# Optimization experiments

Measured on AMD Instinct MI355X. Metric: run time of the kernel, lower is better.

Reference implementation:

```python
import jax, jax.numpy as jnp
import numpy as np

B, DM, H, W = 2, 96, 48, 48
E = 192          # d_expand == d_inner
R, N = 6, 16     # delta_rank, d_state


def conv2d(x, w, b, groups=1, pad=0):
    out = jax.lax.conv_general_dilated(
        x, w, window_strides=(1, 1), padding=[(pad, pad), (pad, pad)],
        dimension_numbers=("NCHW", "OIHW", "NCHW"), feature_group_count=groups)
    return out + b[None, :, None, None]


def setup_inputs() -> dict:
    key = jax.random.key(0)
    ks = jax.random.split(key, 24)
    f = lambda k, shape, s: jax.random.normal(k, shape, jnp.float32) * s
    inp = {
        "x": jax.random.normal(ks[0], (B, DM, H, W), jnp.float32),
        "in_proj_w": f(ks[1], (2 * E, DM), 0.05),
        "conv_w": f(ks[2], (E, 1, 3, 3), 0.2),
        "conv_b": f(ks[3], (E,), 0.1),
        "x_proj_w": f(ks[4], (4, R + 2 * N, E), 0.01),
        "dt_proj_w": f(ks[5], (4, E, R), 0.01),
        "dt_proj_b": jnp.full((4, E), -9.0) + f(ks[6], (4, E), 0.1),
        "A_log": jnp.tile(jnp.log(jnp.arange(1, N + 1, dtype=jnp.float32))[None, None, :], (4, E, 1)),
        "Ds": jnp.ones((4, E), jnp.float32),
        "ln_g": jnp.ones(E, jnp.float32), "ln_b": jnp.zeros(E, jnp.float32),
        "c1_w": f(ks[7], (2 * E, E, 1, 1), 0.05), "c1_b": jnp.zeros(2 * E),
        "bn1_g": jnp.ones(2 * E), "bn1_b": jnp.zeros(2 * E), "bn1_m": jnp.zeros(2 * E), "bn1_v": jnp.ones(2 * E),
        "c2_w": f(ks[8], (2 * E, 1, 3, 3), 0.2), "c2_b": jnp.zeros(2 * E),
        "bn2_g": jnp.ones(2 * E), "bn2_b": jnp.zeros(2 * E), "bn2_m": jnp.zeros(2 * E), "bn2_v": jnp.ones(2 * E),
        "c3_w": f(ks[9], (E // 2, 2 * E, 1, 1), 0.05), "c3_b": jnp.zeros(E // 2),
        "se1_w": f(ks[10], (E // 4, E // 2), 0.1), "se1_b": jnp.zeros(E // 4),
        "se2_w": f(ks[11], (E // 2, E // 4), 0.1), "se2_b": jnp.zeros(E // 2),
    }
    return inp


def reference(x, in_proj_w, conv_w, conv_b, x_proj_w, dt_proj_w, dt_proj_b,
              A_log, Ds, ln_g, ln_b,
              c1_w, c1_b, bn1_g, bn1_b, bn1_m, bn1_v,
              c2_w, c2_b, bn2_g, bn2_b, bn2_m, bn2_v,
              c3_w, c3_b, se1_w, se1_b, se2_w, se2_b):
    Bs, _, Hs, Ws = x.shape
    L = Hs * Ws
    # in projection (Linear over channel dim), split x/z gates
    xz = jnp.einsum("bchw,oc->bohw", x, in_proj_w)
    xi, z = jnp.split(xz, 2, axis=1)
    # depthwise conv + SiLU
    xi = jax.nn.silu(conv2d(xi, conv_w, conv_b, groups=E, pad=1))
    # ---- selective scan (4-direction cross scan, cumsum formulation) ----
    xf = xi.reshape(Bs, E, L)
    xt = jnp.swapaxes(xi, 2, 3).reshape(Bs, E, L)
    xs = jnp.stack([xf, xf[..., ::-1], xt, xt[..., ::-1]], axis=1)  # [B,4,E,L]
    dbc = jnp.einsum("bkcl,krc->bkrl", xs, x_proj_w)                # [B,4,R+2N,L]
    dlt, b, c = dbc[:, :, :R], dbc[:, :, R:R + N], dbc[:, :, R + N:]
    dlt = jnp.einsum("bkrl,kdr->bkdl", dlt, dt_proj_w) + dt_proj_b[None, :, :, None]
    dlt = jax.nn.softplus(dlt)                                      # [B,4,E,L]
    dA = dlt[..., None] * A_log[None, :, :, None, :]                # [B,4,E,L,N]
    phi = jnp.exp(-jnp.cumsum(dA, axis=3))
    dbx = dlt[..., None] * jnp.swapaxes(b, 2, 3)[:, :, None] * xs[..., None]  # [B,4,E,L,N]
    h = phi * jnp.cumsum(dbx / (phi + 1e-12), axis=3)
    y = jnp.einsum("bkdln,bknl->bkdl", h, c) + Ds[None, :, :, None]  # [B,4,E,L]
    # ---- cross merge ----
    y1 = y[:, 0]
    y2 = y[:, 1, :, ::-1]
    y3 = jnp.swapaxes(y[:, 2].reshape(Bs, E, Ws, Hs), 2, 3).reshape(Bs, E, L)
    y4 = jnp.swapaxes(y[:, 3, :, ::-1].reshape(Bs, E, Ws, Hs), 2, 3).reshape(Bs, E, L)
    ys = (y1 + y2 + y3 + y4).reshape(Bs, E, Hs, Ws)
    # layernorm over channels
    yn = jnp.moveaxis(ys, 1, -1)
    mu = yn.mean(-1, keepdims=True)
    var = yn.var(-1, keepdims=True)
    yn = (yn - mu) / jnp.sqrt(var + 1e-5) * ln_g + ln_b
    u = jnp.moveaxis(yn, -1, 1) * z
    # ---- EFFN ----
    def bn(t, g, bb, m, v):
        return (t - m[None, :, None, None]) / jnp.sqrt(v + 1e-5)[None, :, None, None] * g[None, :, None, None] + bb[None, :, None, None]
    t = jax.nn.relu(bn(conv2d(u, c1_w, c1_b), bn1_g, bn1_b, bn1_m, bn1_v))
    t = jax.nn.relu(bn(conv2d(t, c2_w, c2_b, groups=2 * E, pad=1), bn2_g, bn2_b, bn2_m, bn2_v))
    t = conv2d(t, c3_w, c3_b)
    # squeeze-excitation: t + t * sigmoid(fc(relu(fc(avgpool(t)))))
    s = t.mean((2, 3))
    s = jax.nn.relu(s @ se1_w.T + se1_b)
    s = jax.nn.sigmoid(s @ se2_w.T + se2_b)
    return t + t * s[:, :, None, None]
```

## Files before the change

### kernel.cpp

```cpp
#include <hip/hip_runtime.h>
#include <hip/hip_bf16.h>

#define LTOT 2304
#define ECH  192
#define NCH  16
#define CCH  192
#define SCH  12

__device__ __forceinline__ int permS(int k, int l) {
  if (k == 0) return l;
  if (k == 1) return LTOT - 1 - l;
  int m = (k == 2) ? l : (LTOT - 1 - l);
  return (m % 48) * 48 + (m / 48);
}

__device__ __forceinline__ float sp_fast(float x) {
  float t = __expf(x);
  return (t <= 0.018f) ? t * fmaf(t, fmaf(t, 0.33333334f, -0.5f), 1.f) : log1pf(t);
}

__global__ __launch_bounds__(256) void k1_inproj(const float* __restrict__ x,
                                                 const float* __restrict__ W,
                                                 float* __restrict__ xi_pre,
                                                 float* __restrict__ z) {
  const int l0 = blockIdx.x * 32;
  const int o0 = blockIdx.y * 64;
  const int b  = blockIdx.z;
  __shared__ __align__(16) float xs[96 * 34];
  __shared__ __align__(16) float Wl[96 * 68];
  const int tid = threadIdx.x;
  for (int idx = tid; idx < 96 * 32; idx += 256) {
    int i = idx & 31, cc = idx >> 5;
    xs[cc * 34 + i] = x[(b * 96 + cc) * LTOT + l0 + i];
  }
  for (int idx = tid; idx < 96 * 16; idx += 256) {
    int cc = idx % 96, rq = idx / 96;
    float4 v;
    v.x = W[(o0 + 4 * rq + 0) * 96 + cc];
    v.y = W[(o0 + 4 * rq + 1) * 96 + cc];
    v.z = W[(o0 + 4 * rq + 2) * 96 + cc];
    v.w = W[(o0 + 4 * rq + 3) * 96 + cc];
    *(float4*)&Wl[cc * 68 + 4 * rq] = v;
  }
  __syncthreads();
  const int lane = tid & 63, w = tid >> 6;
  const int jj = lane & 15, rqq = lane >> 4;
  const int rbase = 16 * w + 4 * rqq;
  float acc[2][4];
#pragma unroll
  for (int p = 0; p < 2; ++p)
#pragma unroll
    for (int t = 0; t < 4; ++t) acc[p][t] = 0.f;
#pragma unroll 4
  for (int cc = 0; cc < 96; ++cc) {
    const float4 wv = *(const float4*)&Wl[cc * 68 + rbase];
    const float2 xv = *(const float2*)&xs[cc * 34 + 2 * jj];
    acc[0][0] = fmaf(wv.x, xv.x, acc[0][0]); acc[0][1] = fmaf(wv.y, xv.x, acc[0][1]);
    acc[0][2] = fmaf(wv.z, xv.x, acc[0][2]); acc[0][3] = fmaf(wv.w, xv.x, acc[0][3]);
    acc[1][0] = fmaf(wv.x, xv.y, acc[1][0]); acc[1][1] = fmaf(wv.y, xv.y, acc[1][1]);
    acc[1][2] = fmaf(wv.z, xv.y, acc[1][2]); acc[1][3] = fmaf(wv.w, xv.y, acc[1][3]);
  }
  __syncthreads();
  float* ol = xs;
#pragma unroll
  for (int t = 0; t < 4; ++t) {
    ol[(rbase + t) * 33 + 2 * jj]     = acc[0][t];
    ol[(rbase + t) * 33 + 2 * jj + 1] = acc[1][t];
  }
  __syncthreads();
  for (int idx = tid; idx < 32 * 64; idx += 256) {
    int r = idx & 63, pos = idx >> 6;
    float v = ol[r * 33 + pos];
    int o = o0 + r, l = l0 + pos;
    if (o < ECH) xi_pre[(b * LTOT + l) * ECH + o] = v;
    else         z[(b * LTOT + l) * ECH + (o - ECH)] = v;
  }
}

__global__ __launch_bounds__(256) void k2_dwconv(const float4* __restrict__ xi_pre4,
                                                 const float* __restrict__ cw,
                                                 const float* __restrict__ cb,
                                                 float4* __restrict__ xi4) {
  int g = blockIdx.x * 256 + threadIdx.x;
  if (g >= 2 * LTOT * 48) return;
  int e4 = g % 48; int l = (g / 48) % LTOT; int b = g / (48 * LTOT);
  int h = l / 48, wq = l % 48;
  int e0 = 4 * e4;
  float wt[4][9];
#pragma unroll
  for (int j = 0; j < 4; ++j)
#pragma unroll
    for (int t = 0; t < 9; ++t) wt[j][t] = cw[(e0 + j) * 9 + t];
  float4 acc = *(const float4*)&cb[e0];
#pragma unroll
  for (int kh = 0; kh < 3; ++kh) {
    int hh = h + kh - 1; if (hh < 0 || hh >= 48) continue;
#pragma unroll
    for (int kw = 0; kw < 3; ++kw) {
      int ww = wq + kw - 1; if (ww < 0 || ww >= 48) continue;
      float4 v = xi_pre4[(b * LTOT + hh * 48 + ww) * 48 + e4];
      int t = kh * 3 + kw;
// ... 6 lines not shown
  acc.x = acc.x / (1.f + __expf(-acc.x));
  acc.y = acc.y / (1.f + __expf(-acc.y));
  acc.z = acc.z / (1.f + __expf(-acc.z));
  acc.w = acc.w / (1.f + __expf(-acc.w));
  xi4[g] = acc;
}

__global__ __launch_bounds__(256) void k3_xproj(const float* __restrict__ xi,
                                                const float* __restrict__ xw,
                                                float* __restrict__ dl6g,
                                                float* __restrict__ bT,
                                                float* __restrict__ cT) {
  const int l0 = blockIdx.x * 32;
  const int k  = blockIdx.y;
  const int b  = blockIdx.z;
  __shared__ __align__(16) float xs[96 * 34];
  __shared__ __align__(16) float Wl[192 * 44];
  const int tid = threadIdx.x;
  const float* wsrc = xw + k * 38 * ECH;
  for (int idx = tid; idx < 38 * 192; idx += 256) {
    int r = idx / 192, cc = idx - r * 192;
    Wl[cc * 44 + r] = wsrc[idx];
  }
  const int lane = tid & 63, w = tid >> 6;
  const int jj = lane & 15;
  const int rq = w * 4 + (lane >> 4);
  const int rqc = rq < 9 ? rq : 9;
  const int j0 = 2 * jj;
  float a00 = 0.f, a01 = 0.f, a02 = 0.f, a03 = 0.f;
  float a10 = 0.f, a11 = 0.f, a12 = 0.f, a13 = 0.f;
  for (int kc = 0; kc < 2; ++kc) {
    __syncthreads();
    for (int idx = tid; idx < 32 * 96; idx += 256) {
      int j = idx / 96, cc = idx - j * 96;
      int s = permS(k, l0 + j);
      xs[cc * 34 + j] = xi[(b * LTOT + s) * ECH + kc * 96 + cc];
    }
    __syncthreads();
#pragma unroll 4
    for (int cc = 0; cc < 96; ++cc) {
      const float2 xv = *(const float2*)&xs[cc * 34 + j0];
      const float4 wv = *(const float4*)&Wl[(kc * 96 + cc) * 44 + 4 * rqc];
      a00 = fmaf(wv.x, xv.x, a00); a01 = fmaf(wv.y, xv.x, a01);
      a02 = fmaf(wv.z, xv.x, a02); a03 = fmaf(wv.w, xv.x, a03);
      a10 = fmaf(wv.x, xv.y, a10); a11 = fmaf(wv.y, xv.y, a11);
      a12 = fmaf(wv.z, xv.y, a12); a13 = fmaf(wv.w, xv.y, a13);
    }
  }
  const int bk = b * 4 + k;
  if (rq < 10) {
    float av[2][4] = {{a00, a01, a02, a03}, {a10, a11, a12, a13}};
#pragma unroll
    for (int t = 0; t < 4; ++t) {
      int r = 4 * rq + t;
      if (r >= 38) continue;
#pragma unroll
      for (int p = 0; p < 2; ++p) {
        int j = j0 + p;
        float v = av[p][t];
        if (r < 6)       dl6g[((bk * LTOT) + l0 + j) * 6 + r] = v;
        else if (r < 22) bT[((bk * LTOT) + l0 + j) * NCH + (r - 6)] = v;
        else             cT[((bk * LTOT) + l0 + j) * NCH + (r - 22)] = v;
      }
    }
  }
}

__global__ __launch_bounds__(256) void k4a_scan1(const float* __restrict__ dl6g,
                                                 const float* __restrict__ xi,
                                                 const float* __restrict__ bT,
                                                 const float* __restrict__ Alog,
                                                 const float* __restrict__ dtw,
                                                 const float* __restrict__ dtb,
                                                 float* __restrict__ q,
                                                 float* __restrict__ Ts) {
  const int cb = blockIdx.x;
  const int db = blockIdx.y;
  const int bk = blockIdx.z;
  const int b = bk >> 2, k = bk & 3;
  const int l0 = cb * 48;
  __shared__ __align__(16) float2 sdx[48 * 64];
  __shared__ __align__(16) float  sb[48 * NCH];
  const int tid = threadIdx.x;
  const int dd = tid & 63, cg = tid >> 6;
  const int dg = db * 64 + dd;
  float b6 = dtb[k * ECH + dg];
  float w6[6];
  {
    const float2* d2 = (const float2*)(dtw + (k * ECH + dg) * 6);
    float2 u0 = d2[0], u1 = d2[1], u2 = d2[2];
    w6[0] = u0.x; w6[1] = u0.y; w6[2] = u1.x; w6[3] = u1.y; w6[4] = u2.x; w6[5] = u2.y;
  }
  for (int idx = tid; idx < 48 * NCH; idx += 256) sb[idx] = bT[(bk * LTOT + l0) * NCH + idx];
  for (int e = tid; e < 48 * 64; e += 256) {
    int s = e >> 6;
    const float* d6 = dl6g + (bk * LTOT + l0 + s) * 6;
    float xa = b6;
#pragma unroll
    for (int r = 0; r < 6; ++r) xa = fmaf(w6[r], d6[r], xa);
    float dl = sp_fast(xa);
    int sp = permS(k, l0 + s);
    sdx[s * 64 + dd] = make_float2(dl, dl * xi[(b * LTOT + sp) * ECH + dg]);
  }
  float C1[16], h[16];
#pragma unroll
  for (int n = 0; n < 16; ++n) {
    C1[n] = Alog[(k * ECH + dg) * NCH + n];
    h[n] = 0.f;
  }
  __syncthreads();
  float Tsum = 0.f;
  for (int i = 0; i < SCH; ++i) {
    int j = cg * SCH + i;
    float2 dx = sdx[j * 64 + dd];
    float dl = dx.x;
    float u  = dx.y;
    Tsum += dl;
    const float4* bb4 = (const float4*)(sb + j * NCH);
    float4 q0 = bb4[0], q1 = bb4[1], q2 = bb4[2], q3 = bb4[3];
    float bbl[16] = {q0.x, q0.y, q0.z, q0.w, q1.x, q1.y, q1.z, q1.w,
                     q2.x, q2.y, q2.z, q2.w, q3.x, q3.y, q3.z, q3.w};
    if (dl <= 0.018f) {
#pragma unroll
      for (int n = 0; n < 16; ++n) {
        float xn = C1[n] * dl;
        float e = fmaf(xn, fmaf(xn, fmaf(xn, -(1.f / 6.f), 0.5f), -1.f), 1.f);
        h[n] = fmaf(e, h[n], u * bbl[n]);
      }
    } else {
#pragma unroll
      for (int n = 0; n < 16; ++n) {
        float e = __expf(-C1[n] * dl);
        h[n] = fmaf(e, h[n], u * bbl[n]);
      }
    }
  }
  const int c = cb * 4 + cg;
  float4* qp = (float4*)(q + ((bk * CCH + c) * ECH + dg) * NCH);
  qp[0] = make_float4(h[0], h[1], h[2], h[3]);
  qp[1] = make_float4(h[4], h[5], h[6], h[7]);
  qp[2] = make_float4(h[8], h[9], h[10], h[11]);
  qp[3] = make_float4(h[12], h[13], h[14], h[15]);
  Ts[(bk * CCH + c) * ECH + dg] = Tsum;
}

__global__ __launch_bounds__(256) void k4b_comb(const float* __restrict__ Alog,
                                                const float* __restrict__ Ts,
                                                float* __restrict__ q) {
  const int d  = blockIdx.x;
  const int bk = blockIdx.y;
  const int k  = bk & 3;
  const int tid = threadIdx.x;
  const int n = tid & 15, seg = tid >> 4;
  const float A = Alog[(k * ECH + d) * NCH + n];
  const int c0 = seg * 12;
  const float* tb = Ts + (bk * CCH + c0) * ECH + d;
  float* qp = q + ((bk * CCH + c0) * ECH + d) * NCH + n;
  float qv[12], P[12];
#pragma unroll
  for (int i = 0; i < 12; ++i) qv[i] = qp[i * (ECH * NCH)];
#pragma unroll
  for (int i = 0; i < 12; ++i) {
    float xv = A * tb[i * ECH];
    P[i] = (xv <= 0.05f)
               ? fmaf(xv, fmaf(xv, fmaf(xv, -(1.f / 6.f), 0.5f), -1.f), 1.f)
               : __expf(-xv);
  }
  float hl = 0.f, Pp = 1.f;
#pragma unroll
  for (int i = 0; i < 12; ++i) { hl = fmaf(P[i], hl, qv[i]); Pp *= P[i]; }
  __shared__ float2 comb[16][17];
  comb[seg][n] = make_float2(Pp, hl);
  __syncthreads();
  float H = 0.f;
  for (int s = 0; s < seg; ++s) {
    float2 cb = comb[s][n];
    H = fmaf(cb.x, H, cb.y);
  }
  float h = H;
#pragma unroll
  for (int i = 0; i < 12; ++i) {
    float hp = h;
    h = fmaf(P[i], h, qv[i]);
    qp[i * (ECH * NCH)] = hp;
  }
}

__global__ __launch_bounds__(256) void k4c_scan2(const float* __restrict__ dl6g,
                                                 const float* __restrict__ xi,
                                                 const float* __restrict__ bT,
                                                 const float* __restrict__ cT,
                                                 const float* __restrict__ Alog,
                                                 const float* __restrict__ dtw,
                                                 const float* __restrict__ dtb,
                                                 const float* __restrict__ hin,
                                                 float* __restrict__ ys) {
  const int cb = blockIdx.x;
  const int db = blockIdx.y;
  const int bk = blockIdx.z;
  const int b = bk >> 2, k = bk & 3;
  const int l0 = cb * 48;
  __shared__ __align__(16) float2 sdx[48 * 64];
  __shared__ __align__(16) float  sb[48 * NCH];
  __shared__ __align__(16) float  sc[48 * NCH];
  const int tid = threadIdx.x;
  const int dd = tid & 63, cg = tid >> 6;
  const int dg = db * 64 + dd;
  float b6 = dtb[k * ECH + dg];
  float w6[6];
  {
    const float2* d2 = (const float2*)(dtw + (k * ECH + dg) * 6);
    float2 u0 = d2[0], u1 = d2[1], u2 = d2[2];
    w6[0] = u0.x; w6[1] = u0.y; w6[2] = u1.x; w6[3] = u1.y; w6[4] = u2.x; w6[5] = u2.y;
  }
  for (int idx = tid; idx < 48 * NCH; idx += 256) {
    sb[idx] = bT[(bk * LTOT + l0) * NCH + idx];
    sc[idx] = cT[(bk * LTOT + l0) * NCH + idx];
  }
  for (int e = tid; e < 48 * 64; e += 256) {
    int s = e >> 6;
    const float* d6 = dl6g + (bk * LTOT + l0 + s) * 6;
    float xa = b6;
#pragma unroll
    for (int r = 0; r < 6; ++r) xa = fmaf(w6[r], d6[r], xa);
    float dl = sp_fast(xa);
    int sp = permS(k, l0 + s);
    sdx[s * 64 + dd] = make_float2(dl, dl * xi[(b * LTOT + sp) * ECH + dg]);
  }
  float C1[16], h[16];
  const int c = cb * 4 + cg;
  const float4* hp = (const float4*)(hin + ((bk * CCH + c) * ECH + dg) * NCH);
  {
    float4 h0 = hp[0], h1 = hp[1], h2 = hp[2], h3 = hp[3];
    h[0]=h0.x; h[1]=h0.y; h[2]=h0.z; h[3]=h0.w;
    h[4]=h1.x; h[5]=h1.y; h[6]=h1.z; h[7]=h1.w;
    h[8]=h2.x; h[9]=h2.y; h[10]=h2.z; h[11]=h2.w;
    h[12]=h3.x; h[13]=h3.y; h[14]=h3.z; h[15]=h3.w;
  }
#pragma unroll
  for (int n = 0; n < 16; ++n) C1[n] = Alog[(k * ECH + dg) * NCH + n];
  __syncthreads();
  for (int i = 0; i < SCH; ++i) {
    int j = cg * SCH + i;
    float2 dx = sdx[j * 64 + dd];
    float dl = dx.x;
    float u  = dx.y;
    const float4* bb4 = (const float4*)(sb + j * NCH);
    float4 q0 = bb4[0], q1 = bb4[1], q2 = bb4[2], q3 = bb4[3];
    float bbl[16] = {q0.x, q0.y, q0.z, q0.w, q1.x, q1.y, q1.z, q1.w,
                     q2.x, q2.y, q2.z, q2.w, q3.x, q3.y, q3.z, q3.w};
    if (dl <= 0.018f) {
#pragma unroll
      for (int n = 0; n < 16; ++n) {
        float xn = C1[n] * dl;
        float e = fmaf(xn, fmaf(xn, fmaf(xn, -(1.f / 6.f), 0.5f), -1.f), 1.f);
        h[n] = fmaf(e, h[n], u * bbl[n]);
      }
    } else {
#pragma unroll
      for (int n = 0; n < 16; ++n) {
        float e = __expf(-C1[n] * dl);
        h[n] = fmaf(e, h[n], u * bbl[n]);
      }
    }
    const float4* cc4 = (const float4*)(sc + j * NCH);
    float4 c0 = cc4[0], c1 = cc4[1], c2 = cc4[2], c3 = cc4[3];
    float ccl[16] = {c0.x, c0.y, c0.z, c0.w, c1.x, c1.y, c1.z, c1.w,
                     c2.x, c2.y, c2.z, c2.w, c3.x, c3.y, c3.z, c3.w};
    float y = 0.f;
#pragma unroll
    for (int n = 0; n < 16; ++n) y = fmaf(h[n], ccl[n], y);
    int sp = permS(k, l0 + j);
    atomicAdd(&ys[(b * LTOT + sp) * ECH + dg], y);
  }
}

__global__ __launch_bounds__(256) void k5_ln(const float* __restrict__ ys,
                                             const float* __restrict__ Ds,
                                             const float* __restrict__ lng,
                                             const float* __restrict__ lnb,
                                             float* __restrict__ zu) {
  int p = blockIdx.x * 4 + (threadIdx.x >> 6);
  int lane = threadIdx.x & 63;
  const float* yp = ys + p * ECH;
  float vd[3], sd[3];
#pragma unroll
  for (int t = 0; t < 3; ++t) {
    int d = lane + t * 64;
    vd[t] = yp[d];
    sd[t] = Ds[d] + Ds[ECH + d] + Ds[2 * ECH + d] + Ds[3 * ECH + d];
  }
  float s1 = vd[0] + vd[1] + vd[2];
  float s2 = sd[0] + sd[1] + sd[2];
#pragma unroll
  for (int off = 32; off > 0; off >>= 1) {
    s1 += __shfl_xor(s1, off, 64);
    s2 += __shfl_xor(s2, off, 64);
  }
  float mean_dot = s1 * (1.f / 192.f);
  float mean_sd  = s2 * (1.f / 192.f);
  float dev[3];
  float ss = 0.f;
#pragma unroll
  for (int t = 0; t < 3; ++t) {
    dev[t] = (vd[t] - mean_dot) + (sd[t] - mean_sd);
    ss = fmaf(dev[t], dev[t], ss);
  }
#pragma unroll
  for (int off = 32; off > 0; off >>= 1) ss += __shfl_xor(ss, off, 64);
  float rstd = 1.f / sqrtf(ss * (1.f / 192.f) + 1e-5f);
#pragma unroll
  for (int t = 0; t < 3; ++t) {
    int d = lane + t * 64;
    float yn = (dev[t] * rstd) * lng[d] + lnb[d];
    zu[p * ECH + d] = yn * zu[p * ECH + d];
  }
}

__global__ __launch_bounds__(256) void k6_c1(const float* __restrict__ u,
                                             const float* __restrict__ W,
                                             const float* __restrict__ c1b,
                                             const float* __restrict__ g1,
                                             const float* __restrict__ b1,
                                             const float* __restrict__ m1,
                                             const float* __restrict__ v1,
                                             float* __restrict__ t1,
                                             float* __restrict__ se) {
  const int l0 = blockIdx.x * 32;
  const int o0 = blockIdx.y * 64;
// ... 159 lines not shown
}

__global__ __launch_bounds__(256) void k9_out(const float* __restrict__ t3,
                                              const float* __restrict__ se,
                                              const float* __restrict__ w1,
                                              const float* __restrict__ sb1,
                                              const float* __restrict__ w2,
                                              const float* __restrict__ sb2,
                                              float* __restrict__ out) {
  __shared__ float sm[192];
  __shared__ float s1[96];
  __shared__ float smul[192];
  int t = threadIdx.x;
  if (t < 192) sm[t] = se[t] * (1.f / 2304.f);
  __syncthreads();
  if (t < 96) {
    int b = t / 48, i = t % 48;
    float a = sb1[i];
#pragma unroll 4
    for (int m = 0; m < 96; ++m) a = fmaf(w1[i * 96 + m], sm[b * 96 + m], a);
    s1[t] = fmaxf(a, 0.f);
  }
  __syncthreads();
  if (t < 192) {
    int b = t / 96, j = t % 96;
    float a = sb2[j];
#pragma unroll 4
    for (int i = 0; i < 48; ++i) a = fmaf(w2[j * 48 + i], s1[b * 48 + i], a);
    smul[t] = 1.f + 1.f / (1.f + __expf(-a));
  }
  __syncthreads();
  int g = blockIdx.x * 256 + t;
  if (g < 2 * 96 * LTOT) out[g] = t3[g] * smul[g / LTOT];
}

extern "C" void kernel_launch(void* const* d_in, const int* in_sizes, int n_in,
                              void* d_out, int out_size, void* d_ws, size_t ws_size,
                              hipStream_t stream) {
  const float* x     = (const float*)d_in[0];
  const float* inw   = (const float*)d_in[1];
  const float* convw = (const float*)d_in[2];
  const float* convb = (const float*)d_in[3];
  const float* xpw   = (const float*)d_in[4];
  const float* dtw   = (const float*)d_in[5];
  const float* dtb   = (const float*)d_in[6];
  const float* Alog  = (const float*)d_in[7];
  const float* Ds    = (const float*)d_in[8];
  const float* lng   = (const float*)d_in[9];
  const float* lnb   = (const float*)d_in[10];
  const float* c1w   = (const float*)d_in[11];
  const float* c1b   = (const float*)d_in[12];
  const float* bn1g  = (const float*)d_in[13];
  const float* bn1b  = (const float*)d_in[14];
  const float* bn1m  = (const float*)d_in[15];
  const float* bn1v  = (const float*)d_in[16];
  const float* c2w   = (const float*)d_in[17];
  const float* c2b   = (const float*)d_in[18];
  const float* bn2g  = (const float*)d_in[19];
  const float* bn2b  = (const float*)d_in[20];
  const float* bn2m  = (const float*)d_in[21];
  const float* bn2v  = (const float*)d_in[22];
  const float* c3w   = (const float*)d_in[23];
  const float* c3b   = (const float*)d_in[24];
  const float* se1w  = (const float*)d_in[25];
  const float* se1b  = (const float*)d_in[26];
  const float* se2w  = (const float*)d_in[27];
  const float* se2b  = (const float*)d_in[28];

  float* ws = (float*)d_ws;
  float* xi_pre = ws;
  float* z      = ws + 884736;
  float* xi     = ws + 1769472;
  float* dl6g   = ws + 2654208;
  float* bT     = ws + 2764800;
  float* cT     = ws + 3354624;
  float* q      = ws + 3944448;
  float* Ts     = ws + 13381632;
  float* se     = ws + 13676544;
  float* ys     = ws + 13676736;
  float* t1 = q;
  float* t2 = q + 1769472;
  float* t3 = q + 3538944;

  hipMemsetAsync(ys, 0, 884736 * sizeof(float), stream);

  k1_inproj<<<dim3(72, 6, 2), 256, 0, stream>>>(x, inw, xi_pre, z);
  k2_dwconv<<<864, 256, 0, stream>>>((const float4*)xi_pre, convw, convb, (float4*)xi);
  k3_xproj<<<dim3(72, 4, 2), 256, 0, stream>>>(xi, xpw, dl6g, bT, cT);
  k4a_scan1<<<dim3(48, 3, 8), 256, 0, stream>>>(dl6g, xi, bT, Alog, dtw, dtb, q, Ts);
  k4b_comb<<<dim3(192, 8), 256, 0, stream>>>(Alog, Ts, q);
  k4c_scan2<<<dim3(48, 3, 8), 256, 0, stream>>>(dl6g, xi, bT, cT, Alog, dtw, dtb, q, ys);
  k5_ln<<<1152, 256, 0, stream>>>(ys, Ds, lng, lnb, z);
  k6_c1<<<dim3(72, 6, 2), 256, 0, stream>>>(z, c1w, c1b, bn1g, bn1b, bn1m, bn1v, t1, se);
  k7_dw2<<<1728, 256, 0, stream>>>(t1, c2w, c2b, bn2g, bn2b, bn2m, bn2v, t2);
  k8_c3<<<dim3(72, 3, 2), 256, 0, stream>>>(t2, c3w, c3b, t3, se);
  k9_out<<<1728, 256, 0, stream>>>(t3, se, se1w, se1b, se2w, se2b, (float*)d_out);
}
```

Measured before the change: 291.7 us.

## Fuse all stages into one cooperative persistent kernel with grid syncs

Replaces the eleven-kernel launch chain with a single cooperative persistent kernel that walks every stage in grid-stride loops separated by grid-wide barriers. The goal is to remove per-launch overhead and the gaps between kernels, and it also zeroes the ys buffer inside the kernel instead of issuing a memset. The scan chunking changes from 192 chunks of 12 to 144 chunks of 16 steps, processed in two halves through shared memory. Grid syncs cost time of their own, the grid is capped at 1024 blocks, and the multi-kernel path remains as a fallback if the cooperative launch fails.

```diff
diff --git a/kernel.cpp b/kernel.cpp
--- a/kernel.cpp
+++ b/kernel.cpp
@@ -1,11 +1,15 @@
 #include <hip/hip_runtime.h>
 #include <hip/hip_bf16.h>
+#include <hip/hip_cooperative_groups.h>
+
+namespace cg = cooperative_groups;
 
 #define LTOT 2304
 #define ECH  192
 #define NCH  16
 #define CCH  192
 #define SCH  12
+#define MCCH 144
 
 __device__ __forceinline__ int permS(int k, int l) {
   if (k == 0) return l;
@@ -17,6 +21,614 @@
 __device__ __forceinline__ float sp_fast(float x) {
   float t = __expf(x);
   return (t <= 0.018f) ? t * fmaf(t, fmaf(t, 0.33333334f, -0.5f), 1.f) : log1pf(t);
+}
+
+struct MParams {
+  const float *x, *inw, *convw, *convb, *xpw, *dtw, *dtb, *Alog, *Ds, *lng, *lnb;
+  const float *c1w, *c1b, *bn1g, *bn1b, *bn1m, *bn1v;
+  const float *c2w, *c2b, *bn2g, *bn2b, *bn2m, *bn2v;
+  const float *c3w, *c3b, *se1w, *se1b, *se2w, *se2b;
+  float *xi_pre, *z, *xi, *dl6g, *bT, *cT, *q, *Ts, *se, *ys, *out;
+};
+
+__global__ __launch_bounds__(256, 4) void mega(MParams P) {
+  cg::grid_group gridg = cg::this_grid();
+  __shared__ __align__(16) unsigned char smem[39168];
+  const int tid = threadIdx.x;
+  const int bid = blockIdx.x;
+  const int nbl = gridDim.x;
+  const int lane = tid & 63, wv_ = tid >> 6;
+  const int jj = lane & 15, rqq = lane >> 4;
+
+  if (bid == 0 && tid < 192) P.se[tid] = 0.f;
+  {
+    float* xs = (float*)smem;
+    float* Wl = (float*)smem + 96 * 34;
+    const int rbase = 16 * wv_ + 4 * rqq;
+    for (int u = bid; u < 864; u += nbl) {
+      int b = u / 432, rem = u - b * 432;
+      int oy = rem / 72, lb = rem - oy * 72;
+      int l0 = lb * 32, o0 = oy * 64;
+      for (int idx = tid; idx < 96 * 32; idx += 256) {
+        int i = idx & 31, cc = idx >> 5;
+        xs[cc * 34 + i] = P.x[(b * 96 + cc) * LTOT + l0 + i];
+      }
+      for (int idx = tid; idx < 96 * 16; idx += 256) {
+        int cc = idx % 96, rq = idx / 96;
+        float4 v;
+        v.x = P.inw[(o0 + 4 * rq + 0) * 96 + cc];
+        v.y = P.inw[(o0 + 4 * rq + 1) * 96 + cc];
+        v.z = P.inw[(o0 + 4 * rq + 2) * 96 + cc];
+        v.w = P.inw[(o0 + 4 * rq + 3) * 96 + cc];
+        *(float4*)&Wl[cc * 68 + 4 * rq] = v;
+      }
+      __syncthreads();
+      float acc[2][4];
+#pragma unroll
+      for (int p = 0; p < 2; ++p)
+#pragma unroll
+        for (int t = 0; t < 4; ++t) acc[p][t] = 0.f;
+#pragma unroll 4
+      for (int cc = 0; cc < 96; ++cc) {
+        const float4 wv = *(const float4*)&Wl[cc * 68 + rbase];
+        const float2 xv = *(const float2*)&xs[cc * 34 + 2 * jj];
+        acc[0][0] = fmaf(wv.x, xv.x, acc[0][0]); acc[0][1] = fmaf(wv.y, xv.x, acc[0][1]);
+        acc[0][2] = fmaf(wv.z, xv.x, acc[0][2]); acc[0][3] = fmaf(wv.w, xv.x, acc[0][3]);
+        acc[1][0] = fmaf(wv.x, xv.y, acc[1][0]); acc[1][1] = fmaf(wv.y, xv.y, acc[1][1]);
+        acc[1][2] = fmaf(wv.z, xv.y, acc[1][2]); acc[1][3] = fmaf(wv.w, xv.y, acc[1][3]);
+      }
+      __syncthreads();
+      float* ol = xs;
+#pragma unroll
+      for (int t = 0; t < 4; ++t) {
+        ol[(rbase + t) * 33 + 2 * jj]     = acc[0][t];
+        ol[(rbase + t) * 33 + 2 * jj + 1] = acc[1][t];
+      }
+      __syncthreads();
+      for (int idx = tid; idx < 32 * 64; idx += 256) {
+        int r = idx & 63, pos = idx >> 6;
+        float v = ol[r * 33 + pos];
+        int o = o0 + r, l = l0 + pos;
+        if (o < ECH) P.xi_pre[(b * LTOT + l) * ECH + o] = v;
+        else         P.z[(b * LTOT + l) * ECH + (o - ECH)] = v;
+      }
+      __syncthreads();
+    }
+  }
+  gridg.sync();
+
+  {
+    const float4* src4 = (const float4*)P.xi_pre;
+    float4* dst4 = (float4*)P.xi;
+    for (int v2 = bid; v2 < 864; v2 += nbl) {
+      int g = v2 * 256 + tid;
+      int e4 = g % 48; int l = (g / 48) % LTOT; int b = g / (48 * LTOT);
+      int h = l / 48, wq = l % 48;
+      int e0 = 4 * e4;
+      float wt[4][9];
+#pragma unroll
+      for (int j2 = 0; j2 < 4; ++j2)
+#pragma unroll
+        for (int t = 0; t < 9; ++t) wt[j2][t] = P.convw[(e0 + j2) * 9 + t];
+      float4 acc = *(const float4*)&P.convb[e0];
+#pragma unroll
+      for (int kh = 0; kh < 3; ++kh) {
+        int hh = h + kh - 1; if (hh < 0 || hh >= 48) continue;
+#pragma unroll
+        for (int kw = 0; kw < 3; ++kw) {
+          int ww = wq + kw - 1; if (ww < 0 || ww >= 48) continue;
+          float4 v = src4[(b * LTOT + hh * 48 + ww) * 48 + e4];
+          int t = kh * 3 + kw;
+          acc.x = fmaf(wt[0][t], v.x, acc.x);
+          acc.y = fmaf(wt[1][t], v.y, acc.y);
+          acc.z = fmaf(wt[2][t], v.z, acc.z);
+          acc.w = fmaf(wt[3][t], v.w, acc.w);
+        }
+      }
+      acc.x = acc.x / (1.f + __expf(-acc.x));
+      acc.y = acc.y / (1.f + __expf(-acc.y));
+      acc.z = acc.z / (1.f + __expf(-acc.z));
+      acc.w = acc.w / (1.f + __expf(-acc.w));
+      dst4[g] = acc;
+    }
+  }
+  gridg.sync();
+
+  {
+    for (int i = bid * 256 + tid; i < 221184; i += nbl * 256)
+      ((float4*)P.ys)[i] = make_float4(0.f, 0.f, 0.f, 0.f);
+    float* xs = (float*)smem;
+    float* Wl = (float*)smem + 96 * 34;
+    for (int u = bid; u < 576; u += nbl) {
+      int b = u / 288, rem = u - b * 288;
+      int k = rem / 72, lb = rem - k * 72;
+      int l0 = lb * 32;
+      const int rq = wv_ * 4 + rqq;
+      const int rqc = rq < 9 ? rq : 9;
+      const int j0 = 2 * jj;
+      float a00 = 0.f, a01 = 0.f, a02 = 0.f, a03 = 0.f;
+      float a10 = 0.f, a11 = 0.f, a12 = 0.f, a13 = 0.f;
+      for (int kc = 0; kc < 2; ++kc) {
+        __syncthreads();
+        for (int idx = tid; idx < 32 * 96; idx += 256) {
+          int j = idx / 96, cc = idx - j * 96;
+          int s = permS(k, l0 + j);
+          xs[cc * 34 + j] = P.xi[(b * LTOT + s) * ECH + kc * 96 + cc];
+        }
+        for (int idx = tid; idx < 38 * 96; idx += 256) {
+          int r = idx / 96, cc = idx - r * 96;
+          Wl[cc * 44 + r] = P.xpw[(k * 38 + r) * ECH + kc * 96 + cc];
+        }
+        __syncthreads();
+#pragma unroll 4
+        for (int cc = 0; cc < 96; ++cc) {
+          const float2 xv = *(const float2*)&xs[cc * 34 + j0];
+          const float4 wvv = *(const float4*)&Wl[cc * 44 + 4 * rqc];
+          a00 = fmaf(wvv.x, xv.x, a00); a01 = fmaf(wvv.y, xv.x, a01);
+          a02 = fmaf(wvv.z, xv.x, a02); a03 = fmaf(wvv.w, xv.x, a03);
+          a10 = fmaf(wvv.x, xv.y, a10); a11 = fmaf(wvv.y, xv.y, a11);
+          a12 = fmaf(wvv.z, xv.y, a12); a13 = fmaf(wvv.w, xv.y, a13);
+        }
+      }
+      const int bk = b * 4 + k;
+      if (rq < 10) {
+        float av[2][4] = {{a00, a01, a02, a03}, {a10, a11, a12, a13}};
+#pragma unroll
+        for (int t = 0; t < 4; ++t) {
+          int r = 4 * rq + t;
+          if (r >= 38) continue;
+#pragma unroll
+          for (int p = 0; p < 2; ++p) {
+            int j = j0 + p;
+            float v = av[p][t];
+            if (r < 6)       P.dl6g[((bk * LTOT) + l0 + j) * 6 + r] = v;
+            else if (r < 22) P.bT[((bk * LTOT) + l0 + j) * NCH + (r - 6)] = v;
+            else             P.cT[((bk * LTOT) + l0 + j) * NCH + (r - 22)] = v;
+          }
+        }
+      }
+      __syncthreads();
+    }
+  }
+  gridg.sync();
+
+  {
+    float*  sb  = (float*)smem;
+    float2* sdx = (float2*)((float*)smem + 1024);
+    for (int u = bid; u < 864; u += nbl) {
+      int bk = u / 108, r1 = u - bk * 108;
+      int db = r1 / 36, lb = r1 - db * 36;
+      int b = bk >> 2, k = bk & 3;
+      int l0 = lb * 64;
+      int dd = lane, cgw = wv_;
+      int dg = db * 64 + dd;
+      float b6 = P.dtb[k * ECH + dg];
+      float w6[6];
+      {
+        const float2* d2 = (const float2*)(P.dtw + (k * ECH + dg) * 6);
+        float2 u0 = d2[0], u1 = d2[1], u2 = d2[2];
+        w6[0] = u0.x; w6[1] = u0.y; w6[2] = u1.x; w6[3] = u1.y; w6[4] = u2.x; w6[5] = u2.y;
+      }
+      for (int idx = tid; idx < 64 * NCH; idx += 256)
+        sb[idx] = P.bT[(bk * LTOT + l0) * NCH + idx];
+      float C1[16], h[16];
+#pragma unroll
+      for (int n = 0; n < 16; ++n) {
+        C1[n] = P.Alog[(k * ECH + dg) * NCH + n];
+        h[n] = 0.f;
+      }
+      float Tsum = 0.f;
+      for (int hf = 0; hf < 2; ++hf) {
+        __syncthreads();
+        for (int e = tid; e < 32 * 64; e += 256) {
+          int s = e >> 6;
+          int j = (s >> 3) * 16 + hf * 8 + (s & 7);
+          const float* d6 = P.dl6g + (bk * LTOT + l0 + j) * 6;
+          float xa = b6;
+#pragma unroll
+          for (int r = 0; r < 6; ++r) xa = fmaf(w6[r], d6[r], xa);
+          float dl = sp_fast(xa);
+          int sp = permS(k, l0 + j);
+          sdx[s * 64 + dd] = make_float2(dl, dl * P.xi[(b * LTOT + sp) * ECH + dg]);
+        }
+        __syncthreads();
+        for (int i = 0; i < 8; ++i) {
+          int j = cgw * 16 + hf * 8 + i;
+          float2 dx = sdx[(cgw * 8 + i) * 64 + dd];
+          float dl = dx.x, uu = dx.y;
+          Tsum += dl;
+          const float4* bb4 = (const float4*)(sb + j * NCH);
+          float4 q0 = bb4[0], q1 = bb4[1], q2 = bb4[2], q3 = bb4[3];
+          float bbl[16] = {q0.x, q0.y, q0.z, q0.w, q1.x, q1.y, q1.z, q1.w,
+                           q2.x, q2.y, q2.z, q2.w, q3.x, q3.y, q3.z, q3.w};
+          if (dl <= 0.018f) {
+#pragma unroll
+            for (int n = 0; n < 16; ++n) {
+              float xn = C1[n] * dl;
+              float e = fmaf(xn, fmaf(xn, fmaf(xn, -(1.f / 6.f), 0.5f), -1.f), 1.f);
+              h[n] = fmaf(e, h[n], uu * bbl[n]);
+            }
+          } else {
+#pragma unroll
+            for (int n = 0; n < 16; ++n) {
+              float e = __expf(-C1[n] * dl);
+              h[n] = fmaf(e, h[n], uu * bbl[n]);
+            }
+          }
+        }
+      }
+      int c = lb * 4 + cgw;
+      float4* qp = (float4*)(P.q + ((bk * MCCH + c) * ECH + dg) * NCH);
+      qp[0] = make_float4(h[0], h[1], h[2], h[3]);
+      qp[1] = make_float4(h[4], h[5], h[6], h[7]);
+      qp[2] = make_float4(h[8], h[9], h[10], h[11]);
+      qp[3] = make_float4(h[12], h[13], h[14], h[15]);
+      P.Ts[(bk * MCCH + c) * ECH + dg] = Tsum;
+      __syncthreads();
+    }
+  }
+  gridg.sync();
+
+  {
+    float2 (*comb)[17] = (float2(*)[17])smem;
+    for (int u = bid; u < 768; u += nbl) {
+      int bk = u / 96, dp = u - bk * 96;
+      int k = bk & 3;
+      for (int dloc = 0; dloc < 2; ++dloc) {
+        int d = dp * 2 + dloc;
+        int n = tid & 15, seg = tid >> 4;
+        float A = P.Alog[(k * ECH + d) * NCH + n];
+        int c0 = seg * 9;
+        const float* tb = P.Ts + (bk * MCCH + c0) * ECH + d;
+        float* qp = P.q + ((bk * MCCH + c0) * ECH + d) * NCH + n;
+        float qv[9], Pl[9];
+#pragma unroll
+        for (int i = 0; i < 9; ++i) qv[i] = qp[i * (ECH * NCH)];
+#pragma unroll
+        for (int i = 0; i < 9; ++i) {
+          float xv = A * tb[i * ECH];
+          Pl[i] = (xv <= 0.05f)
+                      ? fmaf(xv, fmaf(xv, fmaf(xv, -(1.f / 6.f), 0.5f), -1.f), 1.f)
+                      : __expf(-xv);
+        }
+        float hl = 0.f, Pp = 1.f;
+#pragma unroll
+        for (int i = 0; i < 9; ++i) { hl = fmaf(Pl[i], hl, qv[i]); Pp *= Pl[i]; }
+        comb[seg][n] = make_float2(Pp, hl);
+        __syncthreads();
+        float H = 0.f;
+        for (int s2 = 0; s2 < seg; ++s2) {
+          float2 cb = comb[s2][n];
+          H = fmaf(cb.x, H, cb.y);
+        }
+        float h = H;
+#pragma unroll
+        for (int i = 0; i < 9; ++i) {
+          float hp = h;
+          h = fmaf(Pl[i], h, qv[i]);
+          qp[i * (ECH * NCH)] = hp;
+        }
+        __syncthreads();
+      }
+    }
+  }
+  gridg.sync();
+
+  {
+    float*  sb  = (float*)smem;
+    float*  sc  = (float*)smem + 1024;
+    float2* sdx = (float2*)((float*)smem + 2048);
+    for (int u = bid; u < 864; u += nbl) {
+      int bk = u / 108, r1 = u - bk * 108;
+      int db = r1 / 36, lb = r1 - db * 36;
+      int b = bk >> 2, k = bk & 3;
+      int l0 = lb * 64;
+      int dd = lane, cgw = wv_;
+      int dg = db * 64 + dd;
+      float b6 = P.dtb[k * ECH + dg];
+      float w6[6];
+      {
+        const float2* d2 = (const float2*)(P.dtw + (k * ECH + dg) * 6);
+        float2 u0 = d2[0], u1 = d2[1], u2 = d2[2];
+        w6[0] = u0.x; w6[1] = u0.y; w6[2] = u1.x; w6[3] = u1.y; w6[4] = u2.x; w6[5] = u2.y;
+      }
+      for (int idx = tid; idx < 64 * NCH; idx += 256) {
+        sb[idx] = P.bT[(bk * LTOT + l0) * NCH + idx];
+        sc[idx] = P.cT[(bk * LTOT + l0) * NCH + idx];
+      }
+      int c = lb * 4 + cgw;
+      float C1[16], h[16];
+      const float4* hp4 = (const float4*)(P.q + ((bk * MCCH + c) * ECH + dg) * NCH);
+      {
+        float4 h0 = hp4[0], h1 = hp4[1], h2 = hp4[2], h3 = hp4[3];
+        h[0]=h0.x; h[1]=h0.y; h[2]=h0.z; h[3]=h0.w;
+        h[4]=h1.x; h[5]=h1.y; h[6]=h1.z; h[7]=h1.w;
+        h[8]=h2.x; h[9]=h2.y; h[10]=h2.z; h[11]=h2.w;
+        h[12]=h3.x; h[13]=h3.y; h[14]=h3.z; h[15]=h3.w;
+      }
+#pragma unroll
+      for (int n = 0; n < 16; ++n) C1[n] = P.Alog[(k * ECH + dg) * NCH + n];
+      for (int hf = 0; hf < 2; ++hf) {
+        __syncthreads();
+        for (int e = tid; e < 32 * 64; e += 256) {
+          int s = e >> 6;
+          int j = (s >> 3) * 16 + hf * 8 + (s & 7);
+          const float* d6 = P.dl6g + (bk * LTOT + l0 + j) * 6;
+          float xa = b6;
+#pragma unroll
+          for (int r = 0; r < 6; ++r) xa = fmaf(w6[r], d6[r], xa);
+          float dl = sp_fast(xa);
+          int sp = permS(k, l0 + j);
+          sdx[s * 64 + dd] = make_float2(dl, dl * P.xi[(b * LTOT + sp) * ECH + dg]);
+        }
+        __syncthreads();
+        for (int i = 0; i < 8; ++i) {
+          int j = cgw * 16 + hf * 8 + i;
+          float2 dx = sdx[(cgw * 8 + i) * 64 + dd];
+          float dl = dx.x, uu = dx.y;
+          const float4* bb4 = (const float4*)(sb + j * NCH);
+          float4 q0 = bb4[0], q1 = bb4[1], q2 = bb4[2], q3 = bb4[3];
+          float bbl[16] = {q0.x, q0.y, q0.z, q0.w, q1.x, q1.y, q1.z, q1.w,
+                           q2.x, q2.y, q2.z, q2.w, q3.x, q3.y, q3.z, q3.w};
+          if (dl <= 0.018f) {
+#pragma unroll
+            for (int n = 0; n < 16; ++n) {
+              float xn = C1[n] * dl;
+              float e = fmaf(xn, fmaf(xn, fmaf(xn, -(1.f / 6.f), 0.5f), -1.f), 1.f);
+              h[n] = fmaf(e, h[n], uu * bbl[n]);
+            }
+          } else {
+#pragma unroll
+            for (int n = 0; n < 16; ++n) {
+              float e = __expf(-C1[n] * dl);
+              h[n] = fmaf(e, h[n], uu * bbl[n]);
+            }
+          }
+          const float4* cc4 = (const float4*)(sc + j * NCH);
+          float4 c0v = cc4[0], c1v = cc4[1], c2v = cc4[2], c3v = cc4[3];
+          float ccl[16] = {c0v.x, c0v.y, c0v.z, c0v.w, c1v.x, c1v.y, c1v.z, c1v.w,
+                           c2v.x, c2v.y, c2v.z, c2v.w, c3v.x, c3v.y, c3v.z, c3v.w};
+          float y = 0.f;
+#pragma unroll
+          for (int n = 0; n < 16; ++n) y = fmaf(h[n], ccl[n], y);
+          int sp = permS(k, j + l0);
+          atomicAdd(&P.ys[(b * LTOT + sp) * ECH + dg], y);
+        }
+      }
+      __syncthreads();
+    }
+  }
+  gridg.sync();
+
+  {
+    for (int v2 = bid; v2 < 1152; v2 += nbl) {
+      int p = v2 * 4 + wv_;
+      const float* yp = P.ys + p * ECH;
+      float vd[3], sd[3];
+#pragma unroll
+      for (int t = 0; t < 3; ++t) {
+        int d = lane + t * 64;
+        vd[t] = yp[d];
+        sd[t] = P.Ds[d] + P.Ds[ECH + d] + P.Ds[2 * ECH + d] + P.Ds[3 * ECH + d];
+      }
+      float s1 = vd[0] + vd[1] + vd[2];
+      float s2 = sd[0] + sd[1] + sd[2];
+#pragma unroll
+      for (int off = 32; off > 0; off >>= 1) {
+        s1 += __shfl_xor(s1, off, 64);
+        s2 += __shfl_xor(s2, off, 64);
+      }
+      float mean_dot = s1 * (1.f / 192.f);
+      float mean_sd  = s2 * (1.f / 192.f);
+      float dev[3];
+      float ss = 0.f;
+#pragma unroll
+      for (int t = 0; t < 3; ++t) {
+        dev[t] = (vd[t] - mean_dot) + (sd[t] - mean_sd);
+        ss = fmaf(dev[t], dev[t], ss);
+      }
+#pragma unroll
+      for (int off = 32; off > 0; off >>= 1) ss += __shfl_xor(ss, off, 64);
+      float rstd = 1.f / sqrtf(ss * (1.f / 192.f) + 1e-5f);
+#pragma unroll
+      for (int t = 0; t < 3; ++t) {
+        int d = lane + t * 64;
+        float yn = (dev[t] * rstd) * P.lng[d] + P.lnb[d];
+        P.z[p * ECH + d] = yn * P.z[p * ECH + d];
+      }
+    }
+  }
+  gridg.sync();
+
+  {
+    float* xs = (float*)smem;
+    float* Wl = (float*)smem + 96 * 34;
+    float* t1 = P.q;
+    const int rbase = 16 * wv_ + 4 * rqq;
+    for (int u = bid; u < 864; u += nbl) {
+      int b = u / 432, rem = u - b * 432;
+      int oy = rem / 72, lb = rem - oy * 72;
+      int l0 = lb * 32, o0 = oy * 64;
+      float acc[2][4];
+#pragma unroll
+      for (int p = 0; p < 2; ++p)
+#pragma unroll
+        for (int t = 0; t < 4; ++t) acc[p][t] = 0.f;
+      for (int kc = 0; kc < 2; ++kc) {
+        __syncthreads();
+        for (int idx = tid; idx < 32 * 96; idx += 256) {
+          int cc = idx % 96, i = idx / 96;
+          xs[cc * 34 + i] = P.z[(b * LTOT + l0 + i) * ECH + kc * 96 + cc];
+        }
+        for (int idx = tid; idx < 96 * 16; idx += 256) {
+          int cc = idx % 96, rq = idx / 96;
+          float4 v;
+          v.x = P.c1w[(o0 + 4 * rq + 0) * ECH + kc * 96 + cc];
+          v.y = P.c1w[(o0 + 4 * rq + 1) * ECH + kc * 96 + cc];
+          v.z = P.c1w[(o0 + 4 * rq + 2) * ECH + kc * 96 + cc];
+          v.w = P.c1w[(o0 + 4 * rq + 3) * ECH + kc * 96 + cc];
+          *(float4*)&Wl[cc * 68 + 4 * rq] = v;
+        }
+        __syncthreads();
+#pragma unroll 4
+        for (int cc = 0; cc < 96; ++cc) {
+          const float4 wv = *(const float4*)&Wl[cc * 68 + rbase];
+          const float2 xv = *(const float2*)&xs[cc * 34 + 2 * jj];
+          acc[0][0] = fmaf(wv.x, xv.x, acc[0][0]); acc[0][1] = fmaf(wv.y, xv.x, acc[0][1]);
+          acc[0][2] = fmaf(wv.z, xv.x, acc[0][2]); acc[0][3] = fmaf(wv.w, xv.x, acc[0][3]);
+          acc[1][0] = fmaf(wv.x, xv.y, acc[1][0]); acc[1][1] = fmaf(wv.y, xv.y, acc[1][1]);
+          acc[1][2] = fmaf(wv.z, xv.y, acc[1][2]); acc[1][3] = fmaf(wv.w, xv.y, acc[1][3]);
+        }
+      }
+#pragma unroll
+      for (int t = 0; t < 4; ++t) {
+        int o = o0 + rbase + t;
+        float sc2 = P.bn1g[o] / sqrtf(P.bn1v[o] + 1e-5f);
+        float bias = (P.c1b[o] - P.bn1m[o]) * sc2 + P.bn1b[o];
+#pragma unroll
+        for (int p = 0; p < 2; ++p) acc[p][t] = fmaxf(fmaf(acc[p][t], sc2, bias), 0.f);
+      }
+      __syncthreads();
+      float* ol = xs;
+#pragma unroll
+      for (int t = 0; t < 4; ++t) {
+        ol[(rbase + t) * 33 + 2 * jj]     = acc[0][t];
+        ol[(rbase + t) * 33 + 2 * jj + 1] = acc[1][t];
+      }
+      __syncthreads();
+      for (int idx = tid; idx < 32 * 64; idx += 256) {
+        int pos = idx & 31, r = idx >> 5;
+        t1[(b * 384 + o0 + r) * LTOT + l0 + pos] = ol[r * 33 + pos];
+      }
+      __syncthreads();
+    }
+  }
+  gridg.sync();
+
+  {
+    const float* t1 = P.q;
+    float* t2 = P.q + 1769472;
+    for (int v2 = bid; v2 < 1728; v2 += nbl) {
+      int g = v2 * 256 + tid;
+      int p = g % 576; int o = (g / 576) % 384; int b = g / (576 * 384);
+      int l0 = 4 * p; int h = l0 / 48; int wq0 = l0 % 48;
+      const float* src = t1 + (b * 384 + o) * LTOT;
+      float wt[9];
+#pragma unroll
+      for (int t = 0; t < 9; ++t) wt[t] = P.c2w[o * 9 + t];
+      float bias0 = P.c2b[o];
+      float4 a = make_float4(bias0, bias0, bias0, bias0);
+#pragma unroll
+      for (int kh = 0; kh < 3; ++kh) {
+        int hh = h + kh - 1; if (hh < 0 || hh >= 48) continue;
+        const float* row = src + hh * 48;
+        float4 c = *(const float4*)(row + wq0);
+        float lft = (wq0 > 0)  ? row[wq0 - 1] : 0.f;
+        float rgt = (wq0 < 44) ? row[wq0 + 4] : 0.f;
+        float w0 = wt[kh * 3], w1 = wt[kh * 3 + 1], w2 = wt[kh * 3 + 2];
+        a.x = fmaf(w0, lft, fmaf(w1, c.x, fmaf(w2, c.y, a.x)));
+        a.y = fmaf(w0, c.x, fmaf(w1, c.y, fmaf(w2, c.z, a.y)));
+        a.z = fmaf(w0, c.y, fmaf(w1, c.z, fmaf(w2, c.w, a.z)));
+        a.w = fmaf(w0, c.z, fmaf(w1, c.w, fmaf(w2, rgt, a.w)));
+      }
+      float sc2 = P.bn2g[o] / sqrtf(P.bn2v[o] + 1e-5f);
+      float bs = (0.f - P.bn2m[o]) * sc2 + P.bn2b[o];
+      a.x = fmaxf(fmaf(a.x, sc2, bs), 0.f);
+      a.y = fmaxf(fmaf(a.y, sc2, bs), 0.f);
+      a.z = fmaxf(fmaf(a.z, sc2, bs), 0.f);
+      a.w = fmaxf(fmaf(a.w, sc2, bs), 0.f);
+      *(float4*)(t2 + (b * 384 + o) * LTOT + l0) = a;
+    }
+  }
+  gridg.sync();
+
+  {
+    float* xs = (float*)smem;
+    float* Wl = (float*)smem + 96 * 34;
+    const float* t2 = P.q + 1769472;
+    float* t3 = P.q + 3538944;
+    const int rloc = 8 * wv_ + 2 * rqq;
+    for (int u = bid; u < 432; u += nbl) {
+      int b = u / 216, rem = u - b * 216;
+      int ry = rem / 72, lb = rem - ry * 72;
+      int l0 = lb * 32, r0 = ry * 32;
+      float acc[2][2];
+      acc[0][0] = acc[0][1] = acc[1][0] = acc[1][1] = 0.f;
+      for (int kc = 0; kc < 4; ++kc) {
+        __syncthreads();
+        for (int idx = tid; idx < 96 * 32; idx += 256) {
+          int i = idx & 31, cc = idx >> 5;
+          xs[cc * 34 + i] = t2[(b * 384 + kc * 96 + cc) * LTOT + l0 + i];
+        }
+        for (int idx = tid; idx < 32 * 96; idx += 256) {
+          int r = idx / 96, cc = idx - r * 96;
+          Wl[cc * 34 + r] = P.c3w[(r0 + r) * 384 + kc * 96 + cc];
+        }
+        __syncthreads();
+#pragma unroll 4
+        for (int cc = 0; cc < 96; ++cc) {
+          const float2 wv = *(const float2*)&Wl[cc * 34 + rloc];
+          const float2 xv = *(const float2*)&xs[cc * 34 + 2 * jj];
+          acc[0][0] = fmaf(wv.x, xv.x, acc[0][0]); acc[0][1] = fmaf(wv.y, xv.x, acc[0][1]);
+          acc[1][0] = fmaf(wv.x, xv.y, acc[1][0]); acc[1][1] = fmaf(wv.y, xv.y, acc[1][1]);
+        }
+      }
+      {
+        float b0 = P.c3b[r0 + rloc], b1v = P.c3b[r0 + rloc + 1];
+        acc[0][0] += b0; acc[1][0] += b0; acc[0][1] += b1v; acc[1][1] += b1v;
+      }
+#pragma unroll
+      for (int t = 0; t < 2; ++t) {
+        float v = acc[0][t] + acc[1][t];
+        v += __shfl_xor(v, 1); v += __shfl_xor(v, 2);
+        v += __shfl_xor(v, 4); v += __shfl_xor(v, 8);
+        if (jj == 0) atomicAdd(&P.se[b * 96 + r0 + rloc + t], v);
+      }
+      __syncthreads();
+      float* ol = xs;
+#pragma unroll
+      for (int t = 0; t < 2; ++t) {
+        ol[(rloc + t) * 33 + 2 * jj]     = acc[0][t];
+        ol[(rloc + t) * 33 + 2 * jj + 1] = acc[1][t];
+      }
+      __syncthreads();
+      for (int idx = tid; idx < 32 * 32; idx += 256) {
+        int pos = idx & 31, r = idx >> 5;
+        t3[(b * 96 + r0 + r) * LTOT + l0 + pos] = ol[r * 33 + pos];
+      }
+      __syncthreads();
+    }
+  }
+  gridg.sync();
+
+  {
+    float* sm   = (float*)smem;
+    float* s1b  = sm + 192;
+    float* smul = s1b + 96;
+    const float* t3 = P.q + 3538944;
+    if (tid < 192) sm[tid] = P.se[tid] * (1.f / 2304.f);
+    __syncthreads();
+    if (tid < 96) {
+      int b = tid / 48, i = tid % 48;
+      float a = P.se1b[i];
+#pragma unroll 4
+      for (int m = 0; m < 96; ++m) a = fmaf(P.se1w[i * 96 + m], sm[b * 96 + m], a);
+      s1b[tid] = fmaxf(a, 0.f);
+    }
+    __syncthreads();
+    if (tid < 192) {
+      int b = tid / 96, j = tid % 96;
+      float a = P.se2b[j];
+#pragma unroll 4
+      for (int i = 0; i < 48; ++i) a = fmaf(P.se2w[j * 48 + i], s1b[b * 48 + i], a);
+      smul[tid] = 1.f + 1.f / (1.f + __expf(-a));
+    }
+    __syncthreads();
+    for (int v2 = bid; v2 < 1728; v2 += nbl) {
+      int g = v2 * 256 + tid;
+      P.out[g] = t3[g] * smul[g / LTOT];
+    }
+  }
 }
 
 __global__ __launch_bounds__(256) void k1_inproj(const float* __restrict__ x,
@@ -189,7 +801,7 @@
   __shared__ __align__(16) float2 sdx[48 * 64];
   __shared__ __align__(16) float  sb[48 * NCH];
   const int tid = threadIdx.x;
-  const int dd = tid & 63, cg = tid >> 6;
+  const int dd = tid & 63, cg2 = tid >> 6;
   const int dg = db * 64 + dd;
   float b6 = dtb[k * ECH + dg];
   float w6[6];
@@ -218,10 +830,9 @@
   __syncthreads();
   float Tsum = 0.f;
   for (int i = 0; i < SCH; ++i) {
-    int j = cg * SCH + i;
+    int j = cg2 * SCH + i;
     float2 dx = sdx[j * 64 + dd];
-    float dl = dx.x;
-    float u  = dx.y;
+    float dl = dx.x, u = dx.y;
     Tsum += dl;
     const float4* bb4 = (const float4*)(sb + j * NCH);
     float4 q0 = bb4[0], q1 = bb4[1], q2 = bb4[2], q3 = bb4[3];
@@ -242,7 +853,7 @@
       }
     }
   }
-  const int c = cb * 4 + cg;
+  const int c = cb * 4 + cg2;
   float4* qp = (float4*)(q + ((bk * CCH + c) * ECH + dg) * NCH);
   qp[0] = make_float4(h[0], h[1], h[2], h[3]);
   qp[1] = make_float4(h[4], h[5], h[6], h[7]);
@@ -311,7 +922,7 @@
   __shared__ __align__(16) float  sb[48 * NCH];
   __shared__ __align__(16) float  sc[48 * NCH];
   const int tid = threadIdx.x;
-  const int dd = tid & 63, cg = tid >> 6;
+  const int dd = tid & 63, cg2 = tid >> 6;
   const int dg = db * 64 + dd;
   float b6 = dtb[k * ECH + dg];
   float w6[6];
@@ -335,7 +946,7 @@
     sdx[s * 64 + dd] = make_float2(dl, dl * xi[(b * LTOT + sp) * ECH + dg]);
   }
   float C1[16], h[16];
-  const int c = cb * 4 + cg;
+  const int c = cb * 4 + cg2;
   const float4* hp = (const float4*)(hin + ((bk * CCH + c) * ECH + dg) * NCH);
   {
     float4 h0 = hp[0], h1 = hp[1], h2 = hp[2], h3 = hp[3];
@@ -348,10 +959,9 @@
   for (int n = 0; n < 16; ++n) C1[n] = Alog[(k * ECH + dg) * NCH + n];
   __syncthreads();
   for (int i = 0; i < SCH; ++i) {
-    int j = cg * SCH + i;
+    int j = cg2 * SCH + i;
     float2 dx = sdx[j * 64 + dd];
-    float dl = dx.x;
-    float u  = dx.y;
+    float dl = dx.x, u = dx.y;
     const float4* bb4 = (const float4*)(sb + j * NCH);
     float4 q0 = bb4[0], q1 = bb4[1], q2 = bb4[2], q3 = bb4[3];
     float bbl[16] = {q0.x, q0.y, q0.z, q0.w, q1.x, q1.y, q1.z, q1.w,
@@ -677,17 +1287,38 @@
   float* t2 = q + 1769472;
   float* t3 = q + 3538944;
 
-  hipMemsetAsync(ys, 0, 884736 * sizeof(float), stream);
-
-  k1_inproj<<<dim3(72, 6, 2), 256, 0, stream>>>(x, inw, xi_pre, z);
-  k2_dwconv<<<864, 256, 0, stream>>>((const float4*)xi_pre, convw, convb, (float4*)xi);
-  k3_xproj<<<dim3(72, 4, 2), 256, 0, stream>>>(xi, xpw, dl6g, bT, cT);
-  k4a_scan1<<<dim3(48, 3, 8), 256, 0, stream>>>(dl6g, xi, bT, Alog, dtw, dtb, q, Ts);
-  k4b_comb<<<dim3(192, 8), 256, 0, stream>>>(Alog, Ts, q);
-  k4c_scan2<<<dim3(48, 3, 8), 256, 0, stream>>>(dl6g, xi, bT, cT, Alog, dtw, dtb, q, ys);
-  k5_ln<<<1152, 256, 0, stream>>>(ys, Ds, lng, lnb, z);
-  k6_c1<<<dim3(72, 6, 2), 256, 0, stream>>>(z, c1w, c1b, bn1g, bn1b, bn1m, bn1v, t1, se);
-  k7_dw2<<<1728, 256, 0, stream>>>(t1, c2w, c2b, bn2g, bn2b, bn2m, bn2v, t2);
-  k8_c3<<<dim3(72, 3, 2), 256, 0, stream>>>(t2, c3w, c3b, t3, se);
-  k9_out<<<1728, 256, 0, stream>>>(t3, se, se1w, se1b, se2w, se2b, (float*)d_out);
-}
+  MParams Pm;
+  Pm.x = x; Pm.inw = inw; Pm.convw = convw; Pm.convb = convb; Pm.xpw = xpw;
+  Pm.dtw = dtw; Pm.dtb = dtb; Pm.Alog = Alog; Pm.Ds = Ds; Pm.lng = lng; Pm.lnb = lnb;
+  Pm.c1w = c1w; Pm.c1b = c1b; Pm.bn1g = bn1g; Pm.bn1b = bn1b; Pm.bn1m = bn1m; Pm.bn1v = bn1v;
+  Pm.c2w = c2w; Pm.c2b = c2b; Pm.bn2g = bn2g; Pm.bn2b = bn2b; Pm.bn2m = bn2m; Pm.bn2v = bn2v;
+  Pm.c3w = c3w; Pm.c3b = c3b; Pm.se1w = se1w; Pm.se1b = se1b; Pm.se2w = se2w; Pm.se2b = se2b;
+  Pm.xi_pre = xi_pre; Pm.z = z; Pm.xi = xi; Pm.dl6g = dl6g; Pm.bT = bT; Pm.cT = cT;
+  Pm.q = q; Pm.Ts = Ts; Pm.se = se; Pm.ys = ys; Pm.out = (float*)d_out;
+
+  int nb = 0;
+  hipError_t oe = hipOccupancyMaxActiveBlocksPerMultiprocessor(&nb, mega, 256, 0);
+  int grid = (oe == hipSuccess) ? nb * 256 : 0;
+  if (grid > 1024) grid = 1024;
+  bool done = false;
+  if (grid >= 256) {
+    void* args[] = {(void*)&Pm};
+    hipError_t le = hipLaunchCooperativeKernel((const void*)mega, dim3(grid), dim3(256),
+                                               args, 0, stream);
+    done = (le == hipSuccess);
+  }
+  if (!done) {
+    hipMemsetAsync(ys, 0, 884736 * sizeof(float), stream);
+    k1_inproj<<<dim3(72, 6, 2), 256, 0, stream>>>(x, inw, xi_pre, z);
+    k2_dwconv<<<864, 256, 0, stream>>>((const float4*)xi_pre, convw, convb, (float4*)xi);
+    k3_xproj<<<dim3(72, 4, 2), 256, 0, stream>>>(xi, xpw, dl6g, bT, cT);
+    k4a_scan1<<<dim3(48, 3, 8), 256, 0, stream>>>(dl6g, xi, bT, Alog, dtw, dtb, q, Ts);
+    k4b_comb<<<dim3(192, 8), 256, 0, stream>>>(Alog, Ts, q);
+    k4c_scan2<<<dim3(48, 3, 8), 256, 0, stream>>>(dl6g, xi, bT, cT, Alog, dtw, dtb, q, ys);
+    k5_ln<<<1152, 256, 0, stream>>>(ys, Ds, lng, lnb, z);
+    k6_c1<<<dim3(72, 6, 2), 256, 0, stream>>>(z, c1w, c1b, bn1g, bn1b, bn1m, bn1v, t1, se);
+    k7_dw2<<<1728, 256, 0, stream>>>(t1, c2w, c2b, bn2g, bn2b, bn2m, bn2v, t2);
+    k8_c3<<<dim3(72, 3, 2), 256, 0, stream>>>(t2, c3w, c3b, t3, se);
+    k9_out<<<1728, 256, 0, stream>>>(t3, se, se1w, se1b, se2w, se2b, (float*)d_out);
+  }
+}
```

Result: slower. 969.5 us (+232.3%).
